# Kernel tuning notes

Hardware: AMD Instinct MI355X
Metric: run time of the kernel (lower is better)

Reference implementation:

```python
import jax, jax.numpy as jnp
import numpy as np

ZETA = 2            # cosine kernel exponent
N_ATOMS = 32768
N_SUPPORT = 8192
D_FEAT = 256
N_STRUCT = 512      # query structures (row slices)
N_TRAIN = 256       # training structures (column slices)


def setup_inputs() -> dict:
    key = jax.random.key(0)
    k1, k2, k3, k4, k5 = jax.random.split(key, 5)
    power_spectrum = jax.random.normal(k1, (N_ATOMS, D_FEAT), dtype=jnp.float32)
    # CosineKernel stores row-normalized support points
    support = jax.random.normal(k2, (N_SUPPORT, D_FEAT), dtype=jnp.float32)
    support = support / jnp.linalg.norm(support, axis=1, keepdims=True)
    weights = jax.random.normal(k3, (1, N_TRAIN), dtype=jnp.float32) * 0.01
    # contiguous structure slices encoded as sorted segment ids
    row_segments = jnp.sort(jax.random.randint(k4, (N_ATOMS,), 0, N_STRUCT)).astype(jnp.int32)
    col_segments = jnp.sort(jax.random.randint(k5, (N_SUPPORT,), 0, N_TRAIN)).astype(jnp.int32)
    return {
        "power_spectrum": power_spectrum,
        "support": support,
        "weights": weights,
        "row_segments": row_segments,
        "col_segments": col_segments,
    }


def reference(power_spectrum, support, weights, row_segments, col_segments):
    # CosineKernel: normalize query atoms, cosine similarity raised to zeta
    x = power_spectrum / jnp.linalg.norm(power_spectrum, axis=1, keepdims=True)
    k_atom_atom = jnp.matmul(x, support.T) ** ZETA          # [n_atoms, n_support]
    # SumStructureKernel: ragged block-sum over row and column structure slices
    k_rows = jax.ops.segment_sum(k_atom_atom, row_segments, num_segments=N_STRUCT)  # [n_struct, n_support]
    k_struct = jax.ops.segment_sum(k_rows.T, col_segments, num_segments=N_TRAIN).T  # [n_struct, n_train]
    # final energy prediction: k @ weights.T -> [n_struct, 1]
    return jnp.matmul(k_struct, weights.T)
```

## Files before the change

kernel.cpp:

```cpp
#include <hip/hip_runtime.h>

#define D 256
#define NATOMS 32768
#define NSUP 8192
#define NSTRUCT 512
#define NKC 32

typedef __attribute__((ext_vector_type(8))) short short8;
typedef __attribute__((ext_vector_type(4))) float floatx4;

__device__ __forceinline__ unsigned short f2bf(float f) {
    unsigned int u = __float_as_uint(f);
    u += 0x7FFF + ((u >> 16) & 1);
    return (unsigned short)(u >> 16);
}
__device__ __forceinline__ float bf2f(unsigned short h) {
    return __uint_as_float(((unsigned int)h) << 16);
}


__global__ __launch_bounds__(256) void kA_buildM(const float* __restrict__ S,
                                                 const float* __restrict__ weights,
                                                 const int* __restrict__ colseg,
                                                 float* __restrict__ Mpart) {
    const int tid = threadIdx.x;
    const int l = tid & 63, w = tid >> 6;
    const int wid = blockIdx.x * 4 + w;
    const int pair = wid % 36;
    const int kchunk = wid / 36;
    int sa = 0, rem = pair;
    while (rem >= 8 - sa) { rem -= 8 - sa; ++sa; }
    const int sb = sa + rem;
    const int a0 = sa * 32, b0 = sb * 32;
    const int j0 = kchunk * (NSUP / NKC);
    const int q = l >> 4, ln = l & 15;

    floatx4 acc00 = {0.f, 0.f, 0.f, 0.f}, acc01 = acc00, acc10 = acc00, acc11 = acc00;

    for (int ks = 0; ks < (NSUP / NKC) / 32; ++ks) {
        const int jb = j0 + ks * 32 + q * 8;
        float wv[8], a0v[8], a1v[8], b0v[8], b1v[8];
#pragma unroll
        for (int jj = 0; jj < 8; ++jj) {
            const float* row = S + (size_t)(jb + jj) * D;
            wv[jj] = weights[colseg[jb + jj]];
            a0v[jj] = row[a0 + ln];
            a1v[jj] = row[a0 + 16 + ln];
            b0v[jj] = row[b0 + ln];
            b1v[jj] = row[b0 + 16 + ln];
        }
        short8 fa0, fa1, fb0, fb1;
#pragma unroll
        for (int jj = 0; jj < 8; ++jj) {
            fa0[jj] = (short)f2bf(a0v[jj] * wv[jj]);
            fa1[jj] = (short)f2bf(a1v[jj] * wv[jj]);
            fb0[jj] = (short)f2bf(b0v[jj]);
            fb1[jj] = (short)f2bf(b1v[jj]);
        }
        acc00 = __builtin_amdgcn_mfma_f32_16x16x32_bf16(fa0, fb0, acc00, 0, 0, 0);
        acc01 = __builtin_amdgcn_mfma_f32_16x16x32_bf16(fa0, fb1, acc01, 0, 0, 0);
        acc10 = __builtin_amdgcn_mfma_f32_16x16x32_bf16(fa1, fb0, acc10, 0, 0, 0);
        acc11 = __builtin_amdgcn_mfma_f32_16x16x32_bf16(fa1, fb1, acc11, 0, 0, 0);
    }

    float* Mp = Mpart + (size_t)kchunk * (D * D);
#pragma unroll
    for (int r = 0; r < 4; ++r) {
        Mp[(a0 + q * 4 + r) * D + b0 + ln] = acc00[r];
        Mp[(a0 + q * 4 + r) * D + b0 + 16 + ln] = acc01[r];
        Mp[(a0 + 16 + q * 4 + r) * D + b0 + ln] = acc10[r];
        Mp[(a0 + 16 + q * 4 + r) * D + b0 + 16 + ln] = acc11[r];
    }
}

__global__ __launch_bounds__(256) void kB_sumswz(const float* __restrict__ Mpart,
                                                 unsigned short* __restrict__ Mswz,
                                                 float* __restrict__ out) {
    const int t = blockIdx.x * 256 + threadIdx.x;
    if (t < NSTRUCT) out[t] = 0.0f;
    const int l = t & 63, kc = (t >> 6) & 7, q = t >> 9;
    const int row = q * 16 + (l & 15);
    const int col = kc * 32 + (l >> 4) * 8;
    const int sr = row >> 5;
    float v[8] = {0.f, 0.f, 0.f, 0.f, 0.f, 0.f, 0.f, 0.f};
    if (sr <= kc) {
#pragma unroll
        for (int c = 0; c < NKC; ++c) {
            const float* src = &Mpart[(size_t)c * (D * D) + row * D + col];
            float4 u0 = *(const float4*)src;
            float4 u1 = *(const float4*)(src + 4);
            v[0] += u0.x; v[1] += u0.y; v[2] += u0.z; v[3] += u0.w;
            v[4] += u1.x; v[5] += u1.y; v[6] += u1.z; v[7] += u1.w;
        }
    } else {
#pragma unroll
        for (int j = 0; j < 8; ++j) {
            float s = 0.f;
#pragma unroll
            for (int c = 0; c < NKC; ++c)
                s += Mpart[(size_t)c * (D * D) + (col + j) * D + row];
            v[j] = s;
        }
    }
    *(ushort4*)&Mswz[(size_t)t * 8] = make_ushort4(f2bf(v[0]), f2bf(v[1]), f2bf(v[2]), f2bf(v[3]));
    *(ushort4*)&Mswz[(size_t)t * 8 + 4] = make_ushort4(f2bf(v[4]), f2bf(v[5]), f2bf(v[6]), f2bf(v[7]));
}

__global__ __launch_bounds__(256, 4) void k2_quad(const float* __restrict__ P,
                                                  const unsigned short* __restrict__ Mswz,
                                                  const int* __restrict__ rowseg,
                                                  float* __restrict__ out) {
    __shared__ __align__(16) unsigned short Pt[32][264];
    __shared__ float norms[32];
    __shared__ float esh[4][32];
    const int tid = threadIdx.x;
    const int l = tid & 63, w = tid >> 6;
    const int i0 = blockIdx.x * 32;

    short8 bfn[8];
#pragma unroll
    for (int kc = 0; kc < 8; ++kc)
        bfn[kc] = *(const short8*)&Mswz[(size_t)(((w * 4 + 0) * 8 + kc) * 64 + l) * 8];

    float np[8];
#pragma unroll
    for (int i = 0; i < 8; ++i) {
        const int row = w + 4 * i;
        float4 v = *(const float4*)&P[(size_t)(i0 + row) * D + 4 * l];
        np[i] = v.x * v.x + v.y * v.y + v.z * v.z + v.w * v.w;
        *(ushort4*)&Pt[row][4 * l] = make_ushort4(f2bf(v.x), f2bf(v.y), f2bf(v.z), f2bf(v.w));
    }
#pragma unroll
    for (int i = 0; i < 8; ++i) {
        float s = np[i];
#pragma unroll
        for (int off = 1; off < 64; off <<= 1) s += __shfl_xor(s, off);
        if (l == 0) norms[w + 4 * i] = s;
    }
    __syncthreads();

    short8 af[2][8];
#pragma unroll
    for (int g = 0; g < 2; ++g)
#pragma unroll
        for (int kc = 0; kc < 8; ++kc)
            af[g][kc] = *(const short8*)&Pt[g * 16 + (l & 15)][kc * 32 + (l >> 4) * 8];

    float e[2][4] = {};
#pragma unroll
    for (int nt = 0; nt < 4; ++nt) {
        short8 bf[8];
#pragma unroll
        for (int kc = 0; kc < 8; ++kc) bf[kc] = bfn[kc];
        if (nt < 3) {
#pragma unroll
            for (int kc = 0; kc < 8; ++kc)
                bfn[kc] = *(const short8*)&Mswz[(size_t)(((w * 4 + nt + 1) * 8 + kc) * 64 + l) * 8];
        }
        floatx4 acc[2];
        acc[0] = (floatx4){0.f, 0.f, 0.f, 0.f};
        acc[1] = acc[0];
#pragma unroll
        for (int kc = 0; kc < 8; ++kc)
#pragma unroll
            for (int g = 0; g < 2; ++g)
                acc[g] = __builtin_amdgcn_mfma_f32_16x16x32_bf16(af[g][kc], bf[kc], acc[g], 0, 0, 0);
        const int colg = w * 64 + nt * 16 + (l & 15);
#pragma unroll
        for (int g = 0; g < 2; ++g)
#pragma unroll
            for (int r = 0; r < 4; ++r)
                e[g][r] += acc[g][r] * bf2f(Pt[g * 16 + (l >> 4) * 4 + r][colg]);
    }

#pragma unroll
    for (int off = 1; off < 16; off <<= 1)
#pragma unroll
        for (int g = 0; g < 2; ++g)
#pragma unroll
            for (int r = 0; r < 4; ++r) e[g][r] += __shfl_xor(e[g][r], off);

    if ((l & 15) == 0) {
#pragma unroll
        for (int g = 0; g < 2; ++g)
#pragma unroll
            for (int r = 0; r < 4; ++r)
                esh[w][g * 16 + (l >> 4) * 4 + r] = e[g][r];
    }
    __syncthreads();

    if (tid < 32) {
        float val = (esh[0][tid] + esh[1][tid] + esh[2][tid] + esh[3][tid]) / norms[tid];
        const int seg = rowseg[i0 + tid];
#pragma unroll
        for (int off = 1; off < 32; off <<= 1) {
            float v = __shfl_up(val, off);
            int s2 = __shfl_up(seg, off);
            if (tid >= off && s2 == seg) val += v;
        }
        int segnext = __shfl_down(seg, 1);
        if (tid == 31 || segnext != seg) atomicAdd(&out[seg], val);
    }
}

extern "C" void kernel_launch(void* const* d_in, const int* in_sizes, int n_in,
                              void* d_out, int out_size, void* d_ws, size_t ws_size,
                              hipStream_t stream) {
    const float* P = (const float*)d_in[0];
    const float* S = (const float*)d_in[1];
    const float* W = (const float*)d_in[2];
    const int* rowseg = (const int*)d_in[3];
    const int* colseg = (const int*)d_in[4];
    float* out = (float*)d_out;

    float* Mpart = (float*)d_ws;
    unsigned short* Mswz = (unsigned short*)((char*)d_ws + 8388608);

    kA_buildM<<<dim3(288), dim3(256), 0, stream>>>(S, W, colseg, Mpart);
    kB_sumswz<<<dim3(32), dim3(256), 0, stream>>>(Mpart, Mswz, out);
    k2_quad<<<dim3(NATOMS / 32), dim3(256), 0, stream>>>(P, Mswz, rowseg, out);
}
```

Baseline: 111.9 us.

## Double k-split in M build, tile-based mirrored reduction, 64-row quad tiles

The M-matrix build now splits the support dimension into 64 chunks instead of 32, which doubles the number of blocks and spreads the work across more CUs. The reduction kernel now handles one upper-triangular 32x32 tile per block. It sums the partials with coalesced float4 loads, transposes through shared memory, and writes both the tile and its mirror in the swizzled bf16 layout, replacing the strided transposed reads. The quadratic-form kernel processes 64 atoms per block with a 4x4 MFMA accumulator tile, so each M fragment is reused across twice as many rows. In exchange, the reduction reads twice as much partial data, the workspace grows, and register pressure rises (launch bounds drop to 2 blocks per CU).

```diff
diff --git a/kernel.cpp b/kernel.cpp
--- a/kernel.cpp
+++ b/kernel.cpp
@@ -4,7 +4,7 @@
 #define NATOMS 32768
 #define NSUP 8192
 #define NSTRUCT 512
-#define NKC 32
+#define NKC 64
 
 typedef __attribute__((ext_vector_type(8))) short short8;
 typedef __attribute__((ext_vector_type(4))) float floatx4;
@@ -76,62 +76,63 @@
 __global__ __launch_bounds__(256) void kB_sumswz(const float* __restrict__ Mpart,
                                                  unsigned short* __restrict__ Mswz,
                                                  float* __restrict__ out) {
-    const int t = blockIdx.x * 256 + threadIdx.x;
-    if (t < NSTRUCT) out[t] = 0.0f;
-    const int l = t & 63, kc = (t >> 6) & 7, q = t >> 9;
-    const int row = q * 16 + (l & 15);
-    const int col = kc * 32 + (l >> 4) * 8;
-    const int sr = row >> 5;
-    float v[8] = {0.f, 0.f, 0.f, 0.f, 0.f, 0.f, 0.f, 0.f};
-    if (sr <= kc) {
-#pragma unroll
+    __shared__ __align__(16) float sm[32][36];
+    const int t = threadIdx.x;
+    const int p = blockIdx.x;
+    if (p == 0) { out[t] = 0.0f; out[t + 256] = 0.0f; }
+    int sa = 0, rem = p;
+    while (rem >= 8 - sa) { rem -= 8 - sa; ++sa; }
+    const int sb = sa + rem;
+    const int a0 = sa * 32, b0 = sb * 32;
+    {
+        const int rl = t >> 3, fg = t & 7;
+        const float* src = Mpart + (size_t)(a0 + rl) * D + b0 + fg * 4;
+        float4 acc = make_float4(0.f, 0.f, 0.f, 0.f);
+#pragma unroll 16
         for (int c = 0; c < NKC; ++c) {
-            const float* src = &Mpart[(size_t)c * (D * D) + row * D + col];
-            float4 u0 = *(const float4*)src;
-            float4 u1 = *(const float4*)(src + 4);
-            v[0] += u0.x; v[1] += u0.y; v[2] += u0.z; v[3] += u0.w;
-            v[4] += u1.x; v[5] += u1.y; v[6] += u1.z; v[7] += u1.w;
-        }
-    } else {
-#pragma unroll
-        for (int j = 0; j < 8; ++j) {
-            float s = 0.f;
-#pragma unroll
-            for (int c = 0; c < NKC; ++c)
-                s += Mpart[(size_t)c * (D * D) + (col + j) * D + row];
-            v[j] = s;
-        }
-    }
-    *(ushort4*)&Mswz[(size_t)t * 8] = make_ushort4(f2bf(v[0]), f2bf(v[1]), f2bf(v[2]), f2bf(v[3]));
-    *(ushort4*)&Mswz[(size_t)t * 8 + 4] = make_ushort4(f2bf(v[4]), f2bf(v[5]), f2bf(v[6]), f2bf(v[7]));
-}
-
-__global__ __launch_bounds__(256, 4) void k2_quad(const float* __restrict__ P,
+            float4 u = *(const float4*)(src + (size_t)c * (D * D));
+            acc.x += u.x; acc.y += u.y; acc.z += u.z; acc.w += u.w;
+        }
+        *(float4*)&sm[rl][fg * 4] = acc;
+    }
+    __syncthreads();
+
+    const int h = t & 127;
+    const int rl = h >> 2, cg = h & 3;
+    const bool mir = t >= 128;
+    if (mir && sa == sb) return;
+    float v[8];
+#pragma unroll
+    for (int jj = 0; jj < 8; ++jj)
+        v[jj] = mir ? sm[cg * 8 + jj][rl] : sm[rl][cg * 8 + jj];
+    const int r = (mir ? b0 : a0) + rl;
+    const int c = (mir ? a0 : b0) + cg * 8;
+    const size_t base = (size_t)(((r >> 4) * 8 + (c >> 5)) * 64 + ((c >> 3) & 3) * 16 + (r & 15)) * 8;
+    *(ushort4*)&Mswz[base] = make_ushort4(f2bf(v[0]), f2bf(v[1]), f2bf(v[2]), f2bf(v[3]));
+    *(ushort4*)&Mswz[base + 4] = make_ushort4(f2bf(v[4]), f2bf(v[5]), f2bf(v[6]), f2bf(v[7]));
+}
+
+__global__ __launch_bounds__(256, 2) void k2_quad(const float* __restrict__ P,
                                                   const unsigned short* __restrict__ Mswz,
                                                   const int* __restrict__ rowseg,
                                                   float* __restrict__ out) {
-    __shared__ __align__(16) unsigned short Pt[32][264];
-    __shared__ float norms[32];
-    __shared__ float esh[4][32];
+    __shared__ __align__(16) unsigned short Pt[64][264];
+    __shared__ float norms[64];
+    __shared__ float esh[4][64];
     const int tid = threadIdx.x;
     const int l = tid & 63, w = tid >> 6;
-    const int i0 = blockIdx.x * 32;
-
-    short8 bfn[8];
-#pragma unroll
-    for (int kc = 0; kc < 8; ++kc)
-        bfn[kc] = *(const short8*)&Mswz[(size_t)(((w * 4 + 0) * 8 + kc) * 64 + l) * 8];
-
-    float np[8];
-#pragma unroll
-    for (int i = 0; i < 8; ++i) {
+    const int i0 = blockIdx.x * 64;
+
+    float np[16];
+#pragma unroll
+    for (int i = 0; i < 16; ++i) {
         const int row = w + 4 * i;
         float4 v = *(const float4*)&P[(size_t)(i0 + row) * D + 4 * l];
         np[i] = v.x * v.x + v.y * v.y + v.z * v.z + v.w * v.w;
         *(ushort4*)&Pt[row][4 * l] = make_ushort4(f2bf(v.x), f2bf(v.y), f2bf(v.z), f2bf(v.w));
     }
 #pragma unroll
-    for (int i = 0; i < 8; ++i) {
+    for (int i = 0; i < 16; ++i) {
         float s = np[i];
 #pragma unroll
         for (int off = 1; off < 64; off <<= 1) s += __shfl_xor(s, off);
@@ -139,67 +140,66 @@
     }
     __syncthreads();
 
-    short8 af[2][8];
-#pragma unroll
-    for (int g = 0; g < 2; ++g)
-#pragma unroll
-        for (int kc = 0; kc < 8; ++kc)
-            af[g][kc] = *(const short8*)&Pt[g * 16 + (l & 15)][kc * 32 + (l >> 4) * 8];
-
-    float e[2][4] = {};
+    floatx4 acc[4][4];
+#pragma unroll
+    for (int g = 0; g < 4; ++g)
+#pragma unroll
+        for (int nt = 0; nt < 4; ++nt) acc[g][nt] = (floatx4){0.f, 0.f, 0.f, 0.f};
+
+#pragma unroll 2
+    for (int kc = 0; kc < 8; ++kc) {
+        short8 bf[4], af[4];
+#pragma unroll
+        for (int nt = 0; nt < 4; ++nt)
+            bf[nt] = *(const short8*)&Mswz[(size_t)(((w * 4 + nt) * 8 + kc) * 64 + l) * 8];
+#pragma unroll
+        for (int g = 0; g < 4; ++g)
+            af[g] = *(const short8*)&Pt[g * 16 + (l & 15)][kc * 32 + (l >> 4) * 8];
+#pragma unroll
+        for (int g = 0; g < 4; ++g)
+#pragma unroll
+            for (int nt = 0; nt < 4; ++nt)
+                acc[g][nt] = __builtin_amdgcn_mfma_f32_16x16x32_bf16(af[g], bf[nt], acc[g][nt], 0, 0, 0);
+    }
+
+    float e[4][4] = {};
 #pragma unroll
     for (int nt = 0; nt < 4; ++nt) {
-        short8 bf[8];
-#pragma unroll
-        for (int kc = 0; kc < 8; ++kc) bf[kc] = bfn[kc];
-        if (nt < 3) {
-#pragma unroll
-            for (int kc = 0; kc < 8; ++kc)
-                bfn[kc] = *(const short8*)&Mswz[(size_t)(((w * 4 + nt + 1) * 8 + kc) * 64 + l) * 8];
-        }
-        floatx4 acc[2];
-        acc[0] = (floatx4){0.f, 0.f, 0.f, 0.f};
-        acc[1] = acc[0];
-#pragma unroll
-        for (int kc = 0; kc < 8; ++kc)
-#pragma unroll
-            for (int g = 0; g < 2; ++g)
-                acc[g] = __builtin_amdgcn_mfma_f32_16x16x32_bf16(af[g][kc], bf[kc], acc[g], 0, 0, 0);
         const int colg = w * 64 + nt * 16 + (l & 15);
 #pragma unroll
-        for (int g = 0; g < 2; ++g)
+        for (int g = 0; g < 4; ++g)
 #pragma unroll
             for (int r = 0; r < 4; ++r)
-                e[g][r] += acc[g][r] * bf2f(Pt[g * 16 + (l >> 4) * 4 + r][colg]);
+                e[g][r] += acc[g][nt][r] * bf2f(Pt[g * 16 + (l >> 4) * 4 + r][colg]);
     }
 
 #pragma unroll
     for (int off = 1; off < 16; off <<= 1)
 #pragma unroll
-        for (int g = 0; g < 2; ++g)
+        for (int g = 0; g < 4; ++g)
 #pragma unroll
             for (int r = 0; r < 4; ++r) e[g][r] += __shfl_xor(e[g][r], off);
 
     if ((l & 15) == 0) {
 #pragma unroll
-        for (int g = 0; g < 2; ++g)
+        for (int g = 0; g < 4; ++g)
 #pragma unroll
             for (int r = 0; r < 4; ++r)
                 esh[w][g * 16 + (l >> 4) * 4 + r] = e[g][r];
     }
     __syncthreads();
 
-    if (tid < 32) {
+    if (tid < 64) {
         float val = (esh[0][tid] + esh[1][tid] + esh[2][tid] + esh[3][tid]) / norms[tid];
         const int seg = rowseg[i0 + tid];
 #pragma unroll
-        for (int off = 1; off < 32; off <<= 1) {
+        for (int off = 1; off < 64; off <<= 1) {
             float v = __shfl_up(val, off);
             int s2 = __shfl_up(seg, off);
             if (tid >= off && s2 == seg) val += v;
         }
         int segnext = __shfl_down(seg, 1);
-        if (tid == 31 || segnext != seg) atomicAdd(&out[seg], val);
+        if (tid == 63 || segnext != seg) atomicAdd(&out[seg], val);
     }
 }
 
@@ -214,9 +214,9 @@
     float* out = (float*)d_out;
 
     float* Mpart = (float*)d_ws;
-    unsigned short* Mswz = (unsigned short*)((char*)d_ws + 8388608);
-
-    kA_buildM<<<dim3(288), dim3(256), 0, stream>>>(S, W, colseg, Mpart);
-    kB_sumswz<<<dim3(32), dim3(256), 0, stream>>>(Mpart, Mswz, out);
-    k2_quad<<<dim3(NATOMS / 32), dim3(256), 0, stream>>>(P, Mswz, rowseg, out);
-}
+    unsigned short* Mswz = (unsigned short*)((char*)d_ws + (size_t)NKC * D * D * 4);
+
+    kA_buildM<<<dim3(NKC * 36 / 4), dim3(256), 0, stream>>>(S, W, colseg, Mpart);
+    kB_sumswz<<<dim3(36), dim3(256), 0, stream>>>(Mpart, Mswz, out);
+    k2_quad<<<dim3(NATOMS / 64), dim3(256), 0, stream>>>(P, Mswz, rowseg, out);
+}
```

New measurement: 108.4 us. 3.1% less time.
